# Performance work log

Hardware: AMD Instinct MI355X
Metric: run time of the kernel (lower is better)

## Reference

```python
import jax, jax.numpy as jnp
import numpy as np
import math

N, B, T, E = 4, 8, 2, 1024
H, D = 16, 64
S, L = 2048, 1024
NB = N * B

def setup_inputs() -> dict:
    key = jax.random.key(0)
    ks = jax.random.split(key, 10)
    sc = 0.02
    return {
        'hidden_states': jax.random.normal(ks[0], (NB, T, E), jnp.float32),
        'attention_mask': jnp.zeros((NB, 1, 1, S + L + T), jnp.float32),
        'past_prefix_key': jax.random.normal(ks[1], (N, H, S, D), jnp.float32),
        'past_prefix_value': jax.random.normal(ks[2], (N, H, S, D), jnp.float32),
        'past_key': jax.random.normal(ks[3], (NB, H, L, D), jnp.float32),
        'past_value': jax.random.normal(ks[4], (NB, H, L, D), jnp.float32),
        'Wq': jax.random.normal(ks[5], (E, E), jnp.float32) * sc,
        'bq': jnp.zeros((E,), jnp.float32),
        'Wk': jax.random.normal(ks[6], (E, E), jnp.float32) * sc,
        'bk': jnp.zeros((E,), jnp.float32),
        'Wv': jax.random.normal(ks[7], (E, E), jnp.float32) * sc,
        'bv': jnp.zeros((E,), jnp.float32),
    }

def _heads(x):
    # (NB, T, E) -> (NB, H, T, D)
    return x.reshape(NB, T, H, D).transpose(0, 2, 1, 3)

def reference(hidden_states, attention_mask, past_prefix_key, past_prefix_value,
              past_key, past_value, Wq, bq, Wk, bk, Wv, bv):
    scale = 1.0 / math.sqrt(D)
    q = _heads(hidden_states @ Wq.T + bq)   # (NB,H,T,D)
    k_new = _heads(hidden_states @ Wk.T + bk)
    v_new = _heads(hidden_states @ Wv.T + bv)

    # prefix scores: broadcast shared prefix KV across beams
    q_beam = q.reshape(N, B, H, T, D)
    prefix_scores = jnp.einsum('bxhtd,bhsd->bxhts', q_beam, past_prefix_key)
    prefix_scores = prefix_scores.reshape(NB, H, T, S) * scale

    # current KV = cached target prefix + new tokens
    k = jnp.concatenate([past_key, k_new], axis=2)   # (NB,H,L+T,D)
    v = jnp.concatenate([past_value, v_new], axis=2)
    cur_scores = jnp.einsum('bhtd,bhsd->bhts', q, k) * scale

    scores = jnp.concatenate([prefix_scores, cur_scores], axis=-1) + attention_mask
    probs = jax.nn.softmax(scores, axis=-1)          # (NB,H,T,S+L+T)

    prefix_probs = probs[..., :S].reshape(N, B, H, T, S)
    cur_probs = probs[..., S:]
    prefix_ctx = jnp.einsum('bxhts,bhsd->bxhtd', prefix_probs, past_prefix_value)
    prefix_ctx = prefix_ctx.reshape(NB, H, T, D)
    ctx = prefix_ctx + jnp.einsum('bhts,bhsd->bhtd', cur_probs, v)

    # (NB,H,T,D) -> (NB,T,E)
    return ctx.transpose(0, 2, 1, 3).reshape(NB, T, H * D)
```

## Files before the change

### kernel.cpp

```cpp
#include <hip/hip_runtime.h>
#include <hip/hip_bf16.h>

#define NB_  32
#define T_   2
#define E_   1024
#define H_   16
#define D_   64
#define S_   2048
#define L_   1024
#define TOT_ (S_ + L_ + T_)

#define PCH_  16
#define PLEN_ (S_ / PCH_)
#define NT_   8
#define CCH_  8
#define CLEN_ (L_ / CCH_)

#define PFXBLK_ (4 * H_ * PCH_)
#define CURBLK_ (NB_ * H_ * CCH_)
#define PFXU_ PFXBLK_
#define CURU_ CURBLK_

#define LOG2E_ 1.4426950408889634f
#define QS_ (0.125f * LOG2E_)

#define GLOAD_LDS16(g, l) __builtin_amdgcn_global_load_lds( \
    (const __attribute__((address_space(1))) void*)(g), \
    (__attribute__((address_space(3))) void*)(l), 16, 0, 0)

__global__ __launch_bounds__(256) void qkv_kernel(
    const float* __restrict__ hidden,
    const float* __restrict__ Wq, const float* __restrict__ bq,
    const float* __restrict__ Wk, const float* __restrict__ bk,
    const float* __restrict__ Wv, const float* __restrict__ bv,
    float* __restrict__ qT,
    float* __restrict__ knew,
    float* __restrict__ vnew)
{
    __shared__ float ldsT[128 * 65];
    __shared__ float wlds[8 * 128];
    const int tid  = threadIdx.x;
    const int wave = tid >> 6;
    const int lane = tid & 63;
    const int eg0  = blockIdx.x * 8;
    const int mat  = eg0 >> 10;
    const int e0   = eg0 & 1023;
    int c0 = wave * 2;
    c0 = __builtin_amdgcn_readfirstlane(c0);

    const float* W    = (mat == 0) ? Wq : (mat == 1) ? Wk : Wv;
    const float* bias = (mat == 0) ? bq : (mat == 1) ? bk : bv;

    float aA0 = 0.f, aB0 = 0.f, aA1 = 0.f, aB1 = 0.f;

    for (int k0 = 0; k0 < 1024; k0 += 128) {
        __syncthreads();
        #pragma unroll
        for (int i = 0; i < 32; i++) {
            int f = i * 256 + tid;
            int r = f >> 7;
            int c = f & 127;
            ldsT[c * 65 + r] = hidden[r * 1024 + k0 + c];
        }
        {
            int wr = tid >> 5;
            int wc = (tid & 31) * 4;
            *reinterpret_cast<float4*>(&wlds[wr * 128 + wc]) =
                *reinterpret_cast<const float4*>(&W[(size_t)(e0 + wr) * 1024 + k0 + wc]);
        }
        __syncthreads();

        for (int kk = 0; kk < 128; kk += 4) {
            float h0 = ldsT[(kk + 0) * 65 + lane];
            float h1 = ldsT[(kk + 1) * 65 + lane];
            float h2 = ldsT[(kk + 2) * 65 + lane];
            float h3 = ldsT[(kk + 3) * 65 + lane];
            float4 w0 = *reinterpret_cast<const float4*>(&wlds[(c0 + 0) * 128 + kk]);
            float4 w1 = *reinterpret_cast<const float4*>(&wlds[(c0 + 1) * 128 + kk]);
            aA0 = fmaf(h0, w0.x, aA0); aA0 = fmaf(h1, w0.y, aA0);
            aB0 = fmaf(h2, w0.z, aB0); aB0 = fmaf(h3, w0.w, aB0);
            aA1 = fmaf(h0, w1.x, aA1); aA1 = fmaf(h1, w1.y, aA1);
            aB1 = fmaf(h2, w1.z, aB1); aB1 = fmaf(h3, w1.w, aB1);
        }
    }

    const int r = lane;
    #pragma unroll
    for (int j = 0; j < 2; j++) {
        int e_in = e0 + c0 + j;
        float val = ((j == 0) ? (aA0 + aB0) : (aA1 + aB1)) + bias[e_in];
        if (mat == 0) {
            qT[e_in * 64 + r] = val;
        } else {
            int nb = r >> 1, t = r & 1, h = e_in >> 6, d = e_in & 63;
            float* dst = (mat == 1) ? knew : vnew;
            dst[((nb * H_ + h) * T_ + t) * D_ + d] = val;
        }
    }
}

__global__ __launch_bounds__(256) void partial_kernel(
    const float* __restrict__ mask,
    const float* __restrict__ pfx_k,
    const float* __restrict__ pfx_v,
    const float* __restrict__ pk,
    const float* __restrict__ pv,
    const float* __restrict__ qT,
    const float* __restrict__ knew,
    const float* __restrict__ vnew,
    float* __restrict__ cur_ctx,
    float* __restrict__ cur_l,
    float* __restrict__ pfx_ctx,
    float* __restrict__ pfx_l)
{
    __shared__ float smem[4160];
    const int tid = threadIdx.x;

    if (blockIdx.x < PFXBLK_) {
        const int v     = blockIdx.x;
        const int n     = v >> 8;
        const int h     = (v >> 4) & 15;
        const int chunk = v & 15;
        const int wv    = tid >> 6;
        const int lane  = tid & 63;
        const int r     = lane & 15;
        const int c     = lane >> 4;

        float qreg[16];
        const float* qbase = qT + (h * 64 + c * 16) * 64 + (n * 16 + r);
        #pragma unroll
        for (int u = 0; u < 16; u++) qreg[u] = qbase[u * 64] * QS_;

        const size_t pos0 = (size_t)(n * H_ + h) * S_ + chunk * PLEN_;
        const float* kb = pfx_k + pos0 * D_;
        const float* vb = pfx_v + pos0 * D_;
        const float* mrow = mask + (n * 8 + (r >> 1)) * TOT_ + chunk * PLEN_;

        float ctx[16];
        #pragma unroll
        for (int u = 0; u < 16; u++) ctx[u] = 0.f;
        float lsum = 0.f;

        GLOAD_LDS16(kb + tid * 4, &smem[tid * 4]);
        GLOAD_LDS16(vb + tid * 4, &smem[1024 + tid * 4]);

        #pragma unroll 1
        for (int t = 0; t < NT_; t++) {
            const int bufo = (t & 1) * 2048;
            __syncthreads();

            float mreg[4];
            #pragma unroll
            for (int j = 0; j < 4; j++)
                mreg[j] = mrow[t * 16 + wv * 4 + j] * LOG2E_;

            if (t < NT_ - 1) {
                const int nbo = ((t + 1) & 1) * 2048;
                const float* kn = kb + (size_t)(t + 1) * 16 * 64;
                const float* vn = vb + (size_t)(t + 1) * 16 * 64;
                GLOAD_LDS16(kn + tid * 4, &smem[nbo + tid * 4]);
                GLOAD_LDS16(vn + tid * 4, &smem[nbo + 1024 + tid * 4]);
            }

            #pragma unroll
            for (int j = 0; j < 4; j++) {
                const int pp = wv * 4 + j;
                const float4* kq = reinterpret_cast<const float4*>(
                    &smem[bufo + pp * 64 + c * 16]);
                float4 k0 = kq[0], k1 = kq[1], k2 = kq[2], k3 = kq[3];
                float sA = qreg[0]*k0.x;  sA = fmaf(qreg[1],k0.y,sA);
                sA = fmaf(qreg[2],k0.z,sA); sA = fmaf(qreg[3],k0.w,sA);
                float sB = qreg[4]*k1.x;  sB = fmaf(qreg[5],k1.y,sB);
                sB = fmaf(qreg[6],k1.z,sB); sB = fmaf(qreg[7],k1.w,sB);
                float sC = qreg[8]*k2.x;  sC = fmaf(qreg[9],k2.y,sC);
                sC = fmaf(qreg[10],k2.z,sC); sC = fmaf(qreg[11],k2.w,sC);
                float sD = qreg[12]*k3.x; sD = fmaf(qreg[13],k3.y,sD);
                sD = fmaf(qreg[14],k3.z,sD); sD = fmaf(qreg[15],k3.w,sD);
                float s = (sA + sB) + (sC + sD);
                s += __shfl_xor(s, 16, 64);
                s += __shfl_xor(s, 32, 64);
                float e = exp2f(s + mreg[j]);
                lsum += e;
                const float4* vq = reinterpret_cast<const float4*>(
                    &smem[bufo + 1024 + pp * 64 + c * 16]);
                float4 v0 = vq[0], v1 = vq[1], v2 = vq[2], v3 = vq[3];
                ctx[0]  += e * v0.x; ctx[1]  += e * v0.y; ctx[2]  += e * v0.z; ctx[3]  += e * v0.w;
                ctx[4]  += e * v1.x; ctx[5]  += e * v1.y; ctx[6]  += e * v1.z; ctx[7]  += e * v1.w;
                ctx[8]  += e * v2.x; ctx[9]  += e * v2.y; ctx[10] += e * v2.z; ctx[11] += e * v2.w;
                ctx[12] += e * v3.x; ctx[13] += e * v3.y; ctx[14] += e * v3.z; ctx[15] += e * v3.w;
            }
        }

        __syncthreads();
        const int base = wv * 1024 + r * 64 + c * 16;
        #pragma unroll
        for (int u = 0; u < 16; u += 4)
            *reinterpret_cast<float4*>(&smem[base + u]) =
                make_float4(ctx[u], ctx[u+1], ctx[u+2], ctx[u+3]);
        if (c == 0) smem[4096 + wv * 16 + r] = lsum;
        __syncthreads();

        const int pc = (n * H_ + h) * PCH_ + chunk;
        for (int e = tid; e < 1024; e += 256) {
            float s = smem[e] + smem[1024 + e] + smem[2048 + e] + smem[3072 + e];
            pfx_ctx[pc * 1024 + e] = s;
        }
        if (tid < 16) {
            float l = smem[4096 + tid] + smem[4096 + 16 + tid]
                    + smem[4096 + 32 + tid] + smem[4096 + 48 + tid];
            pfx_l[pc * 16 + tid] = l;
        }
    } else {
        const int u     = blockIdx.x - PFXBLK_;
        const int b     = u >> 3;
        const int chunk = u & 7;
        const int nb    = b >> 4;
        const int h     = b & 15;
        const int g     = tid >> 4;
        const int l16   = tid & 15;
        const int d0    = l16 * 4;

        float qf0[4], qf1[4];
        #pragma unroll
        for (int j = 0; j < 4; j++) {
            const float* qb = qT + (h * 64 + d0 + j) * 64 + nb * 2;
            qf0[j] = qb[0] * QS_;
            qf1[j] = qb[1] * QS_;
        }

        const float* pk_b = pk + ((nb * H_ + h) * (size_t)L_) * D_;
        const float* pv_b = pv + ((nb * H_ + h) * (size_t)L_) * D_;
        const float* mrow = mask + nb * TOT_ + S_;

        float l0 = 0.f, l1 = 0.f;
        float a0[4] = {0.f,0.f,0.f,0.f};
        float a1[4] = {0.f,0.f,0.f,0.f};

        const int p0 = chunk * CLEN_ + g;
        float4 kf = *reinterpret_cast<const float4*>(pk_b + (size_t)p0 * D_ + d0);
        float4 vf = *reinterpret_cast<const float4*>(pv_b + (size_t)p0 * D_ + d0);
        float  mv = mrow[p0];

        #pragma unroll
        for (int i = 0; i < 8; i++) {
            float4 kf2, vf2; float m2;
            if (i < 7) {
                int pn = p0 + (i + 1) * 16;
                kf2 = *reinterpret_cast<const float4*>(pk_b + (size_t)pn * D_ + d0);
                vf2 = *reinterpret_cast<const float4*>(pv_b + (size_t)pn * D_ + d0);
                m2  = mrow[pn];
            }
            float s0 = fmaf(qf0[0],kf.x, qf0[1]*kf.y) + fmaf(qf0[2],kf.z, qf0[3]*kf.w);
            float s1 = fmaf(qf1[0],kf.x, qf1[1]*kf.y) + fmaf(qf1[2],kf.z, qf1[3]*kf.w);
            #pragma unroll
            for (int off = 1; off < 16; off <<= 1) {
                s0 += __shfl_xor(s0, off, 64);
                s1 += __shfl_xor(s1, off, 64);
            }
            float mC = mv * LOG2E_;
            float e0 = exp2f(s0 + mC);
            float e1 = exp2f(s1 + mC);
            l0 += e0; l1 += e1;
            a0[0] += e0 * vf.x; a0[1] += e0 * vf.y; a0[2] += e0 * vf.z; a0[3] += e0 * vf.w;
            a1[0] += e1 * vf.x; a1[1] += e1 * vf.y; a1[2] += e1 * vf.z; a1[3] += e1 * vf.w;
            if (i < 7) { kf = kf2; vf = vf2; mv = m2; }
        }

        if (chunk == 7 && g < 2) {
            const float* kn_b = knew + (nb * H_ + h) * (T_ * D_);
            const float* vn_b = vnew + (nb * H_ + h) * (T_ * D_);
            float4 kfn = *reinterpret_cast<const float4*>(kn_b + g * D_ + d0);
            float s0 = fmaf(qf0[0],kfn.x, qf0[1]*kfn.y) + fmaf(qf0[2],kfn.z, qf0[3]*kfn.w);
            float s1 = fmaf(qf1[0],kfn.x, qf1[1]*kfn.y) + fmaf(qf1[2],kfn.z, qf1[3]*kfn.w);
            #pragma unroll
            for (int off = 1; off < 16; off <<= 1) {
                s0 += __shfl_xor(s0, off, 64);
                s1 += __shfl_xor(s1, off, 64);
            }
            float mC = mrow[L_ + g] * LOG2E_;
            float e0 = exp2f(s0 + mC);
            float e1 = exp2f(s1 + mC);
            l0 += e0; l1 += e1;
            float4 vfn = *reinterpret_cast<const float4*>(vn_b + g * D_ + d0);
            a0[0] += e0 * vfn.x; a0[1] += e0 * vfn.y; a0[2] += e0 * vfn.z; a0[3] += e0 * vfn.w;
            a1[0] += e1 * vfn.x; a1[1] += e1 * vfn.y; a1[2] += e1 * vfn.z; a1[3] += e1 * vfn.w;
        }

        #pragma unroll
        for (int j = 0; j < 4; j++) {
            smem[g * 128 + d0 + j]      = a0[j];
            smem[g * 128 + 64 + d0 + j] = a1[j];
        }
        if (l16 == 0) { smem[2048 + g * 2] = l0; smem[2048 + g * 2 + 1] = l1; }
        __syncthreads();

        if (tid < 128) {
            int t = tid >> 6, d = tid & 63;
            float s = 0.f, l = 0.f;
            for (int g2 = 0; g2 < 16; g2++) {
                s += smem[g2 * 128 + t * 64 + d];
                l += smem[2048 + g2 * 2 + t];
            }
            cur_ctx[(u * 2 + t) * 64 + d] = s;
            if (d == 0) cur_l[u * 2 + t] = l;
        }
    }
}

__global__ __launch_bounds__(256) void combine_kernel(
    const float* __restrict__ cur_ctx, const float* __restrict__ cur_l,
    const float* __restrict__ pfx_ctx, const float* __restrict__ pfx_l,
    float* __restrict__ out)
{
    const int row = blockIdx.x >> 2;
    const int qtr = blockIdx.x & 3;
    const int nb  = row >> 1, t = row & 1;
    const int n   = nb >> 3;
    const int r   = (nb & 7) * 2 + t;
    const int e   = qtr * 256 + threadIdx.x;
    const int h   = e >> 6, d = e & 63;
    const int b   = nb * 16 + h;

    float val = 0.f, l = 0.f;
    #pragma unroll
    for (int ch = 0; ch < CCH_; ch++) {
        int cb = (b * CCH_ + ch);
        val += cur_ctx[(cb * 2 + t) * 64 + d];
        l   += cur_l[cb * 2 + t];
    }
    #pragma unroll
    for (int ch = 0; ch < PCH_; ch++) {
        int pc = (n * H_ + h) * PCH_ + ch;
        val += pfx_ctx[pc * 1024 + r * 64 + d];
        l   += pfx_l[pc * 16 + r];
    }
    out[row * 1024 + e] = val / l;
}

extern "C" void kernel_launch(void* const* d_in, const int* in_sizes, int n_in,
                              void* d_out, int out_size, void* d_ws, size_t ws_size,
                              hipStream_t stream) {
    const float* hidden = (const float*)d_in[0];
    const float* mask   = (const float*)d_in[1];
    const float* pfxk   = (const float*)d_in[2];
    const float* pfxv   = (const float*)d_in[3];
    const float* pk     = (const float*)d_in[4];
    const float* pv     = (const float*)d_in[5];
    const float* Wq     = (const float*)d_in[6];
    const float* bq     = (const float*)d_in[7];
    const float* Wk     = (const float*)d_in[8];
    const float* bk     = (const float*)d_in[9];
    const float* Wv     = (const float*)d_in[10];
    const float* bv     = (const float*)d_in[11];

    float* qT      = (float*)d_ws;
    float* knew    = qT + 65536;
    float* vnew    = knew + 65536;
    float* cur_ctx = vnew + 65536;
    float* cur_l   = cur_ctx + 524288;
    float* pfx_ctx = cur_l + 8192;
    float* pfx_l   = pfx_ctx + 1048576;

    qkv_kernel<<<384, 256, 0, stream>>>(hidden, Wq, bq, Wk, bk, Wv, bv,
                                        qT, knew, vnew);
    partial_kernel<<<PFXBLK_ + CURBLK_, 256, 0, stream>>>(
        mask, pfxk, pfxv, pk, pv, qT, knew, vnew,
        cur_ctx, cur_l, pfx_ctx, pfx_l);
    combine_kernel<<<256, 256, 0, stream>>>(cur_ctx, cur_l, pfx_ctx, pfx_l,
                                            (float*)d_out);
}
```

Measured before the change: 104.5 us.

## Merge prefix and cached-KV work into uniform persistent blocks with LDS-staged loads

The prefix attention is split into twice as many shorter chunks. Each block of a fixed 2048-block grid now handles one prefix chunk and then two cached-KV units in a loop, instead of each block doing one kind of work. The cached-KV path switches from per-thread register prefetch to double-buffered async global-to-LDS loads, with the mask values preloaded into registers. The aim is to balance the work per block and improve memory-latency hiding on this bandwidth-bound kernel. In exchange it adds extra barriers and doubles the partial prefix outputs that the combine step must reduce.

Result: slower. 120.4 us (+15.2%).

```diff
diff --git a/kernel.cpp b/kernel.cpp
--- a/kernel.cpp
+++ b/kernel.cpp
@@ -10,16 +10,16 @@
 #define L_   1024
 #define TOT_ (S_ + L_ + T_)
 
-#define PCH_  16
-#define PLEN_ (S_ / PCH_)
-#define NT_   8
+#define PCH_  32
+#define PLEN_ 64
+#define PNT_  4
 #define CCH_  8
-#define CLEN_ (L_ / CCH_)
-
-#define PFXBLK_ (4 * H_ * PCH_)
-#define CURBLK_ (NB_ * H_ * CCH_)
-#define PFXU_ PFXBLK_
-#define CURU_ CURBLK_
+#define CLEN_ 128
+#define CNT_  8
+
+#define PFXU_ (4 * H_ * PCH_)
+#define CURU_ (NB_ * H_ * CCH_)
+#define GRID_ 2048
 
 #define LOG2E_ 1.4426950408889634f
 #define QS_ (0.125f * LOG2E_)
@@ -116,11 +116,11 @@
     __shared__ float smem[4160];
     const int tid = threadIdx.x;
 
-    if (blockIdx.x < PFXBLK_) {
+    {
         const int v     = blockIdx.x;
-        const int n     = v >> 8;
-        const int h     = (v >> 4) & 15;
-        const int chunk = v & 15;
+        const int n     = v >> 9;
+        const int h     = (v >> 5) & 15;
+        const int chunk = v & 31;
         const int wv    = tid >> 6;
         const int lane  = tid & 63;
         const int r     = lane & 15;
@@ -145,7 +145,7 @@
         GLOAD_LDS16(vb + tid * 4, &smem[1024 + tid * 4]);
 
         #pragma unroll 1
-        for (int t = 0; t < NT_; t++) {
+        for (int t = 0; t < PNT_; t++) {
             const int bufo = (t & 1) * 2048;
             __syncthreads();
 
@@ -154,10 +154,10 @@
             for (int j = 0; j < 4; j++)
                 mreg[j] = mrow[t * 16 + wv * 4 + j] * LOG2E_;
 
-            if (t < NT_ - 1) {
+            if (t < PNT_ - 1) {
                 const int nbo = ((t + 1) & 1) * 2048;
-                const float* kn = kb + (size_t)(t + 1) * 16 * 64;
-                const float* vn = vb + (size_t)(t + 1) * 16 * 64;
+                const float* kn = kb + (size_t)(t + 1) * 1024;
+                const float* vn = vb + (size_t)(t + 1) * 1024;
                 GLOAD_LDS16(kn + tid * 4, &smem[nbo + tid * 4]);
                 GLOAD_LDS16(vn + tid * 4, &smem[nbo + 1024 + tid * 4]);
             }
@@ -210,8 +210,11 @@
                     + smem[4096 + 32 + tid] + smem[4096 + 48 + tid];
             pfx_l[pc * 16 + tid] = l;
         }
-    } else {
-        const int u     = blockIdx.x - PFXBLK_;
+    }
+
+    #pragma unroll 1
+    for (int kph = 0; kph < 2; kph++) {
+        const int u     = blockIdx.x + kph * GRID_;
         const int b     = u >> 3;
         const int chunk = u & 7;
         const int nb    = b >> 4;
@@ -228,28 +231,36 @@
             qf1[j] = qb[1] * QS_;
         }
 
-        const float* pk_b = pk + ((nb * H_ + h) * (size_t)L_) * D_;
-        const float* pv_b = pv + ((nb * H_ + h) * (size_t)L_) * D_;
-        const float* mrow = mask + nb * TOT_ + S_;
+        const float* kb = pk + ((nb * H_ + h) * (size_t)L_ + chunk * CLEN_) * D_;
+        const float* vb = pv + ((nb * H_ + h) * (size_t)L_ + chunk * CLEN_) * D_;
+        const float* mrow = mask + nb * TOT_ + S_ + chunk * CLEN_;
+
+        float mreg[8];
+        #pragma unroll
+        for (int t = 0; t < 8; t++) mreg[t] = mrow[t * 16 + g] * LOG2E_;
 
         float l0 = 0.f, l1 = 0.f;
         float a0[4] = {0.f,0.f,0.f,0.f};
         float a1[4] = {0.f,0.f,0.f,0.f};
 
-        const int p0 = chunk * CLEN_ + g;
-        float4 kf = *reinterpret_cast<const float4*>(pk_b + (size_t)p0 * D_ + d0);
-        float4 vf = *reinterpret_cast<const float4*>(pv_b + (size_t)p0 * D_ + d0);
-        float  mv = mrow[p0];
-
-        #pragma unroll
-        for (int i = 0; i < 8; i++) {
-            float4 kf2, vf2; float m2;
-            if (i < 7) {
-                int pn = p0 + (i + 1) * 16;
-                kf2 = *reinterpret_cast<const float4*>(pk_b + (size_t)pn * D_ + d0);
-                vf2 = *reinterpret_cast<const float4*>(pv_b + (size_t)pn * D_ + d0);
-                m2  = mrow[pn];
-            }
+        __syncthreads();
+        GLOAD_LDS16(kb + tid * 4, &smem[tid * 4]);
+        GLOAD_LDS16(vb + tid * 4, &smem[1024 + tid * 4]);
+
+        #pragma unroll 1
+        for (int t = 0; t < CNT_; t++) {
+            const int bufo = (t & 1) * 2048;
+            __syncthreads();
+
+            if (t < CNT_ - 1) {
+                const int nbo = ((t + 1) & 1) * 2048;
+                const float* kn = kb + (size_t)(t + 1) * 1024;
+                const float* vn = vb + (size_t)(t + 1) * 1024;
+                GLOAD_LDS16(kn + tid * 4, &smem[nbo + tid * 4]);
+                GLOAD_LDS16(vn + tid * 4, &smem[nbo + 1024 + tid * 4]);
+            }
+
+            float4 kf = *reinterpret_cast<const float4*>(&smem[bufo + g * 64 + d0]);
             float s0 = fmaf(qf0[0],kf.x, qf0[1]*kf.y) + fmaf(qf0[2],kf.z, qf0[3]*kf.w);
             float s1 = fmaf(qf1[0],kf.x, qf1[1]*kf.y) + fmaf(qf1[2],kf.z, qf1[3]*kf.w);
             #pragma unroll
@@ -257,13 +268,12 @@
                 s0 += __shfl_xor(s0, off, 64);
                 s1 += __shfl_xor(s1, off, 64);
             }
-            float mC = mv * LOG2E_;
-            float e0 = exp2f(s0 + mC);
-            float e1 = exp2f(s1 + mC);
+            float e0 = exp2f(s0 + mreg[t]);
+            float e1 = exp2f(s1 + mreg[t]);
             l0 += e0; l1 += e1;
+            float4 vf = *reinterpret_cast<const float4*>(&smem[bufo + 1024 + g * 64 + d0]);
             a0[0] += e0 * vf.x; a0[1] += e0 * vf.y; a0[2] += e0 * vf.z; a0[3] += e0 * vf.w;
             a1[0] += e1 * vf.x; a1[1] += e1 * vf.y; a1[2] += e1 * vf.z; a1[3] += e1 * vf.w;
-            if (i < 7) { kf = kf2; vf = vf2; mv = m2; }
         }
 
         if (chunk == 7 && g < 2) {
@@ -277,7 +287,7 @@
                 s0 += __shfl_xor(s0, off, 64);
                 s1 += __shfl_xor(s1, off, 64);
             }
-            float mC = mrow[L_ + g] * LOG2E_;
+            float mC = mask[nb * TOT_ + S_ + L_ + g] * LOG2E_;
             float e0 = exp2f(s0 + mC);
             float e1 = exp2f(s1 + mC);
             l0 += e0; l1 += e1;
@@ -286,6 +296,7 @@
             a1[0] += e1 * vfn.x; a1[1] += e1 * vfn.y; a1[2] += e1 * vfn.z; a1[3] += e1 * vfn.w;
         }
 
+        __syncthreads();
         #pragma unroll
         for (int j = 0; j < 4; j++) {
             smem[g * 128 + d0 + j]      = a0[j];
@@ -304,6 +315,7 @@
             cur_ctx[(u * 2 + t) * 64 + d] = s;
             if (d == 0) cur_l[u * 2 + t] = l;
         }
+        __syncthreads();
     }
 }
 
@@ -359,11 +371,11 @@
     float* cur_ctx = vnew + 65536;
     float* cur_l   = cur_ctx + 524288;
     float* pfx_ctx = cur_l + 8192;
-    float* pfx_l   = pfx_ctx + 1048576;
+    float* pfx_l   = pfx_ctx + 2097152;
 
     qkv_kernel<<<384, 256, 0, stream>>>(hidden, Wq, bq, Wk, bk, Wv, bv,
                                         qT, knew, vnew);
-    partial_kernel<<<PFXBLK_ + CURBLK_, 256, 0, stream>>>(
+    partial_kernel<<<GRID_, 256, 0, stream>>>(
         mask, pfxk, pfxv, pk, pv, qT, knew, vnew,
         cur_ctx, cur_l, pfx_ctx, pfx_l);
     combine_kernel<<<256, 256, 0, stream>>>(cur_ctx, cur_l, pfx_ctx, pfx_l,
```
